# Kernel tuning notes

Hardware: AMD Instinct MI355X
Metric: run time of the kernel (lower is better)

## Reference

```python
import jax, jax.numpy as jnp
import numpy as np

H, I, SI, E = 2048, 1408, 5632, 60
B, S = 1, 512


def setup_inputs() -> dict:
    key = jax.random.key(0)
    ks = jax.random.split(key, 9)
    sc = 0.02  # weight init scale for numerical stability
    return {
        "hidden_states": jax.random.normal(ks[0], (B, S, H), dtype=jnp.float32),
        "router_w": jax.random.normal(ks[1], (E, H), dtype=jnp.float32) * sc,
        "gate_w": jax.random.normal(ks[2], (E, I, H), dtype=jnp.float32) * sc,
        "up_w": jax.random.normal(ks[3], (E, I, H), dtype=jnp.float32) * sc,
        "down_w": jax.random.normal(ks[4], (E, H, I), dtype=jnp.float32) * sc,
        "sh_gate_w": jax.random.normal(ks[5], (SI, H), dtype=jnp.float32) * sc,
        "sh_up_w": jax.random.normal(ks[6], (SI, H), dtype=jnp.float32) * sc,
        "sh_down_w": jax.random.normal(ks[7], (H, SI), dtype=jnp.float32) * sc,
        "expert_gate_w": jax.random.normal(ks[8], (1, H), dtype=jnp.float32) * sc,
        "top_k": 4,
    }


NORM_TOPK_PROB = False  # Qwen1.5-MoE config


def reference(hidden_states, router_w, gate_w, up_w, down_w,
              sh_gate_w, sh_up_w, sh_down_w, expert_gate_w, top_k):
    b, s, h = hidden_states.shape
    x = hidden_states.reshape(-1, h)                      # [T, H]

    # --- router: softmax over all experts, then top-k sparse weights ---
    logits = x @ router_w.T                               # [T, E]
    probs = jax.nn.softmax(logits.astype(jnp.float32), axis=-1)
    vals, idx = jax.lax.top_k(probs, top_k)               # [T, k]
    if NORM_TOPK_PROB:
        vals = vals / jnp.sum(vals, axis=-1, keepdims=True)
    # scatter top-k weights back to dense [T, E] (zeros elsewhere)
    onehot = jax.nn.one_hot(idx, E, dtype=probs.dtype)    # [T, k, E]
    w = jnp.einsum('tke,tk->te', onehot, vals).astype(x.dtype)  # [T, E]

    # --- grouped GLU experts (dense-masked faithful reference) ---
    g = jnp.einsum('td,eid->tei', x, gate_w)              # [T, E, I]
    a = jax.nn.silu(g) * jnp.einsum('td,eid->tei', x, up_w)
    moe = jnp.einsum('tei,ehi,te->th', a, down_w, w)      # [T, H]

    # --- shared expert with sigmoid gate ---
    shared = (jax.nn.silu(x @ sh_gate_w.T) * (x @ sh_up_w.T)) @ sh_down_w.T
    shared = jax.nn.sigmoid(x @ expert_gate_w.T) * shared # [T,1]*[T,H]

    return (moe + shared).reshape(b, s, h)
```

## Files before the change

kernel.cpp:

```cpp
#include <hip/hip_runtime.h>
#include <hip/hip_bf16.h>
#include <stdint.h>

#define TOKENS 512
#define HDIM   2048
#define IDIM   1408
#define SIDIM  5632
#define NEXP   60
#define TOPK   4
#define NSLOTS (TOKENS*TOPK)
#define ROWPAD 64

#define VMWAIT(N) asm volatile("s_waitcnt vmcnt(" #N ")" ::: "memory")
#define SBAR()    asm volatile("s_barrier" ::: "memory")

typedef __attribute__((ext_vector_type(8))) short bf16x8;
typedef __attribute__((ext_vector_type(4))) float f32x4;

__device__ __forceinline__ short f2bf(float f){
  uint32_t u = __float_as_uint(f);
  u = (u + 0x7fffu + ((u >> 16) & 1u)) >> 16;
  return (short)(u & 0xffffu);
}

__device__ __forceinline__ bf16x8 pack8(float4 a, float4 b){
  bf16x8 r;
  r[0]=f2bf(a.x); r[1]=f2bf(a.y); r[2]=f2bf(a.z); r[3]=f2bf(a.w);
  r[4]=f2bf(b.x); r[5]=f2bf(b.y); r[6]=f2bf(b.z); r[7]=f2bf(b.w);
  return r;
}

__device__ __forceinline__ bf16x8 as_bf16x8(float4 v){
  union { float4 f; bf16x8 b; } u; u.f = v; return u.b;
}

__device__ __forceinline__ f32x4 zero4(){
  f32x4 z; z[0]=0.f; z[1]=0.f; z[2]=0.f; z[3]=0.f; return z;
}

__device__ __forceinline__ f32x4 mfma16(bf16x8 a, bf16x8 b, f32x4 c){
  return __builtin_amdgcn_mfma_f32_16x16x32_bf16(a, b, c, 0, 0, 0);
}

__device__ __forceinline__ void stage_w(float4* tile, const float* __restrict__ W,
                                        int K, int k0, int tid){
  int l = tid & 63, wv = tid >> 6;
  #pragma unroll
  for (int i=0;i<4;i++){
    int r  = i*16 + wv*4 + (l>>4);
    int lu = ((l & 15) - (r & 15)) & 15;
    const float* src = W + (size_t)r*K + k0 + lu*4;
    float4* dst = tile + (size_t)(i*16 + wv*4)*16;
    __builtin_amdgcn_global_load_lds(
        (const __attribute__((address_space(1))) void*)src,
        (__attribute__((address_space(3))) void*)dst, 16, 0, 0);
  }
}

__device__ __forceinline__ void read_wfrag(const float4* tile, int r, int kq,
                                           bf16x8& b0, bf16x8& b1){
  int rot = r & 15;
  const float4* row = tile + (size_t)r*16;
  float4 f0 = row[(2*kq     + rot) & 15];
  float4 f1 = row[(2*kq + 1 + rot) & 15];
  float4 f2 = row[(2*kq + 8 + rot) & 15];
  float4 f3 = row[(2*kq + 9 + rot) & 15];
  b0 = pack8(f0, f1);
  b1 = pack8(f2, f3);
}

__device__ __forceinline__ void stage_a(float4* tile, const short* __restrict__ Arows,
                                        int K, int k0, int tid){
  int l = tid & 63, wv = tid >> 6;
  #pragma unroll
  for (int j=0;j<2;j++){
    int u0 = wv*128 + j*64;
    int u  = u0 + l;
    int row = u >> 3;
    int lu  = ((u & 7) - (row & 7)) & 7;
    const short* src = Arows + (size_t)row*K + k0 + lu*8;
    __builtin_amdgcn_global_load_lds(
        (const __attribute__((address_space(1))) void*)src,
        (__attribute__((address_space(3))) void*)(tile + u0), 16, 0, 0);
  }
}

__device__ __forceinline__ void read_afrag(const float4* tile, int c16, int kq,
                                           bf16x8* av){
  #pragma unroll
  for (int mf=0; mf<4; mf++){
    int row = c16 + 16*mf;
    const float4* rp = tile + (size_t)row*8;
    av[mf]   = as_bf16x8(rp[(kq     + row) & 7]);
    av[4+mf] = as_bf16x8(rp[(kq + 4 + row) & 7]);
  }
}

__device__ __forceinline__ void swz_decode(bool expert_mode, int& bx, int& by){
  int bid = blockIdx.y * gridDim.x + blockIdx.x;
  int nb  = gridDim.x * gridDim.y;
  int w_  = ((nb & 7) == 0) ? ((bid & 7) * (nb >> 3) + (bid >> 3)) : bid;
  if (expert_mode){ bx = w_ % gridDim.x; by = w_ / gridDim.x; }
  else            { by = w_ % gridDim.y; bx = w_ / gridDim.y; }
}

__global__ __launch_bounds__(64) void router_kernel(
    const float* __restrict__ x, const float* __restrict__ rw,
    const float* __restrict__ egw, int* __restrict__ topk_idx,
    float* __restrict__ topk_w, float* __restrict__ gates,
    int* __restrict__ counts)
{
  int t = blockIdx.x;
  int lane = threadIdx.x;
  const float* xr = x + (size_t)t*HDIM;
  float xv[HDIM/64];
  #pragma unroll
  for (int i=0;i<HDIM/64;i++) xv[i] = xr[lane + 64*i];

  float mylogit = -1e30f;
  for (int e=0;e<NEXP;e++){
    const float* w = rw + (size_t)e*HDIM;
    float acc = 0.f;
    #pragma unroll
    for (int i=0;i<HDIM/64;i++) acc += xv[i]*w[lane+64*i];
    #pragma unroll
    for (int s=32;s>0;s>>=1) acc += __shfl_xor(acc, s);
    if (lane == e) mylogit = acc;
  }
  {
    float acc = 0.f;
    #pragma unroll
    for (int i=0;i<HDIM/64;i++) acc += xv[i]*egw[lane+64*i];
    #pragma unroll
    for (int s=32;s>0;s>>=1) acc += __shfl_xor(acc, s);
    if (lane == 0) gates[t] = 1.f/(1.f + __expf(-acc));
  }
  float m = mylogit;
  #pragma unroll
  for (int s=32;s>0;s>>=1) m = fmaxf(m, __shfl_xor(m, s));
  float p = (lane < NEXP) ? __expf(mylogit - m) : 0.f;
  float sum = p;
  #pragma unroll
  for (int s=32;s>0;s>>=1) sum += __shfl_xor(sum, s);
  float prob = p / sum;
  for (int k=0;k<TOPK;k++){
    float v = prob; int idx = lane;
    #pragma unroll
    for (int s=32;s>0;s>>=1){
      float ov = __shfl_xor(v, s); int oi = __shfl_xor(idx, s);
      if (ov > v || (ov == v && oi < idx)){ v = ov; idx = oi; }
    }
    if (lane == 0){
      topk_idx[t*TOPK+k] = idx;
      topk_w[t*TOPK+k]  = v;
      atomicAdd(&counts[idx], 1);
    }
    if (lane == idx) prob = -1e30f;
  }
}

__global__ void prefix_kernel(const int* __restrict__ counts, int* __restrict__ offsets)
{
  if (threadIdx.x == 0){
    int acc = 0;
    for (int e=0;e<NEXP;e++){ offsets[e] = acc; acc += counts[e]; }
    offsets[NEXP] = acc;
  }
}

__global__ __launch_bounds__(256) void scatter_kernel(
    const float* __restrict__ x, const int* __restrict__ topk_idx,
    const int* __restrict__ offsets, int* __restrict__ fill,
    int* __restrict__ slot_of, __hip_bfloat16* __restrict__ xg,
    __hip_bfloat16* __restrict__ xb)
{
  int t = blockIdx.x, tid = threadIdx.x;
  __shared__ int sl[TOPK];
  if (tid == 0){
    for (int k=0;k<TOPK;k++){
      int e = topk_idx[t*TOPK+k];
      int pos = atomicAdd(&fill[e], 1);
      int s = offsets[e] + pos;
      slot_of[t*TOPK+k] = s;
      sl[k] = s;
    }
  }
  __syncthreads();
  const float4* xr = (const float4*)(x + (size_t)t*HDIM);
  float4 v0 = xr[tid*2], v1 = xr[tid*2+1];
  bf16x8 b = pack8(v0, v1);
  *(bf16x8*)((short*)xb + (size_t)t*HDIM + tid*8) = b;
  #pragma unroll
  for (int k=0;k<TOPK;k++)
    *(bf16x8*)((short*)xg + (size_t)sl[k]*HDIM + tid*8) = b;
}

__global__ __launch_bounds__(256) void gateup_kernel(
    const float* __restrict__ Wg_base, const float* __restrict__ Wu_base,
    const __hip_bfloat16* __restrict__ A, __hip_bfloat16* __restrict__ out,
    const int* __restrict__ offsets, int K, int NI)
{
  extern __shared__ __align__(16) char smem[];
  float4* G0 = (float4*)smem;
  float4* G1 = G0 + 1024;
  float4* U0 = G1 + 1024;
  float4* U1 = U0 + 1024;
  float4* A0 = U1 + 1024;
  float4* A1 = A0 + 512;

  int bx, by;
  swz_decode(offsets != nullptr, bx, by);

  int m_start, m_end;
  const float *Wg = Wg_base, *Wu = Wu_base;
  if (offsets){
    m_start = offsets[by]; m_end = offsets[by+1];
    size_t wo = (size_t)by * NI * K;
    Wg += wo; Wu += wo;
  } else {
    m_start = by * 64; m_end = m_start + 64;
  }
  if (m_start >= m_end) return;

  int tid  = threadIdx.x;
  int lane = tid & 63;
  int wv   = tid >> 6;
  int c16 = lane & 15, kq = lane >> 4;
  int wrow = bx*64 + wv*16 + c16;
  int r    = wv*16 + c16;
  const float* WgT = Wg + (size_t)(bx*64)*K;
  const float* WuT = Wu + (size_t)(bx*64)*K;
  const short* As = (const short*)A;

  for (int m0 = m_start; m0 < m_end; m0 += 64){
    int mrem = m_end - m0;
    const short* Ar = As + (size_t)m0*K;
    f32x4 accg[4], accu[4];
    #pragma unroll
    for (int i=0;i<4;i++){ accg[i] = zero4(); accu[i] = zero4(); }

    stage_w(G0, WgT, K, 0, tid);
    stage_w(U0, WuT, K, 0, tid);
    stage_a(A0, Ar,  K, 0, tid);

    for (int k0 = 0; k0 < K; k0 += 128){
      stage_w(G1, WgT, K, k0+64, tid);
      stage_w(U1, WuT, K, k0+64, tid);
      stage_a(A1, Ar,  K, k0+64, tid);
      VMWAIT(10); SBAR();
      {
        bf16x8 av[8], bg0,bg1,bu0,bu1;
        read_afrag(A0, c16, kq, av);
        read_wfrag(G0, r, kq, bg0, bg1);
        read_wfrag(U0, r, kq, bu0, bu1);
        #pragma unroll
        for (int mf=0; mf<4; mf++){
          accg[mf] = mfma16(av[mf],   bg0, accg[mf]);
          accu[mf] = mfma16(av[mf],   bu0, accu[mf]);
          accg[mf] = mfma16(av[4+mf], bg1, accg[mf]);
          accu[mf] = mfma16(av[4+mf], bu1, accu[mf]);
        }
      }
      SBAR();
      if (k0 + 128 < K){
        stage_w(G0, WgT, K, k0+128, tid);
        stage_w(U0, WuT, K, k0+128, tid);
        stage_a(A0, Ar,  K, k0+128, tid);
        VMWAIT(10);
      } else {
        VMWAIT(0);
      }
      SBAR();
      {
        bf16x8 av[8], bg0,bg1,bu0,bu1;
        read_afrag(A1, c16, kq, av);
        read_wfrag(G1, r, kq, bg0, bg1);
        read_wfrag(U1, r, kq, bu0, bu1);
        #pragma unroll
        for (int mf=0; mf<4; mf++){
          accg[mf] = mfma16(av[mf],   bg0, accg[mf]);
          accu[mf] = mfma16(av[mf],   bu0, accu[mf]);
          accg[mf] = mfma16(av[4+mf], bg1, accg[mf]);
          accu[mf] = mfma16(av[4+mf], bu1, accu[mf]);
        }
      }
      SBAR();
    }

    #pragma unroll
    for (int mf=0; mf<4; mf++){
      #pragma unroll
      for (int j=0;j<4;j++){
        int mrow = mf*16 + kq*4 + j;
        if (mrow < mrem){
          float g = accg[mf][j], u = accu[mf][j];
          float s = g * u / (1.f + __expf(-g));
          ((short*)out)[(size_t)(m0+mrow)*NI + wrow] = f2bf(s);
        }
      }
    }
  }
}

__global__ __launch_bounds__(256) void down_kernel(
    const float* __restrict__ W_base, const __hip_bfloat16* __restrict__ A,
    float* __restrict__ out, const int* __restrict__ offsets, int K, int NH)
{
  extern __shared__ __align__(16) char smem[];
  float4* W0 = (float4*)smem;
  float4* W1 = W0 + 1024;
  float4* A0 = W1 + 1024;
  float4* A1 = A0 + 512;

  int bx, by;
  swz_decode(offsets != nullptr, bx, by);

  int m_start, m_end;
  const float* W = W_base;
  if (offsets){
    m_start = offsets[by]; m_end = offsets[by+1];
    W += (size_t)by * NH * K;
  } else {
    m_start = by * 64; m_end = m_start + 64;
  }
  if (m_start >= m_end) return;

  int tid  = threadIdx.x;
  int lane = tid & 63;
  int wv   = tid >> 6;
  int c16 = lane & 15, kq = lane >> 4;
  int wrow = bx*64 + wv*16 + c16;
  int r    = wv*16 + c16;
  const float* WT = W + (size_t)(bx*64)*K;
  const short* As = (const short*)A;

  for (int m0 = m_start; m0 < m_end; m0 += 64){
    int mrem = m_end - m0;
    const short* Ar = As + (size_t)m0*K;
    f32x4 acc[4];
    #pragma unroll
    for (int i=0;i<4;i++) acc[i] = zero4();

    stage_w(W0, WT, K, 0, tid);
    stage_a(A0, Ar, K, 0, tid);

    for (int k0 = 0; k0 < K; k0 += 128){
      stage_w(W1, WT, K, k0+64, tid);
      stage_a(A1, Ar, K, k0+64, tid);
      VMWAIT(6); SBAR();
      {
        bf16x8 av[8], b0,b1;
        read_afrag(A0, c16, kq, av);
        read_wfrag(W0, r, kq, b0, b1);
        #pragma unroll
        for (int mf=0; mf<4; mf++){
          acc[mf] = mfma16(av[mf],   b0, acc[mf]);
          acc[mf] = mfma16(av[4+mf], b1, acc[mf]);
        }
      }
      SBAR();
      if (k0 + 128 < K){
        stage_w(W0, WT, K, k0+128, tid);
        stage_a(A0, Ar, K, k0+128, tid);
        VMWAIT(6);
      } else {
        VMWAIT(0);
      }
      SBAR();
      {
        bf16x8 av[8], b0,b1;
        read_afrag(A1, c16, kq, av);
        read_wfrag(W1, r, kq, b0, b1);
        #pragma unroll
        for (int mf=0; mf<4; mf++){
          acc[mf] = mfma16(av[mf],   b0, acc[mf]);
          acc[mf] = mfma16(av[4+mf], b1, acc[mf]);
        }
      }
      SBAR();
    }

    #pragma unroll
    for (int mf=0; mf<4; mf++){
      #pragma unroll
      for (int j=0;j<4;j++){
        int mrow = mf*16 + kq*4 + j;
        if (mrow < mrem)
          out[(size_t)(m0+mrow)*NH + wrow] = acc[mf][j];
      }
    }
  }
}

__global__ __launch_bounds__(256) void combine_kernel(
    const float* __restrict__ dslot, const float* __restrict__ shdown,
    const int* __restrict__ slot_of, const float* __restrict__ topw,
    const float* __restrict__ gates, float* __restrict__ out)
{
  int t = blockIdx.x, tid = threadIdx.x;
  int4  sl = ((const int4*)slot_of)[t];
  float4 w = ((const float4*)topw)[t];
  float sg = gates[t];
  const float* r0 = dslot + (size_t)sl.x*HDIM;
  const float* r1 = dslot + (size_t)sl.y*HDIM;
  const float* r2 = dslot + (size_t)sl.z*HDIM;
  const float* r3 = dslot + (size_t)sl.w*HDIM;
  const float* rs = shdown + (size_t)t*HDIM;
  float* o = out + (size_t)t*HDIM;
  #pragma unroll
  for (int it=0; it<HDIM/(256*4); ++it){
    int h = (tid + it*256) * 4;
    float4 a0 = *(const float4*)(r0+h);
    float4 a1 = *(const float4*)(r1+h);
    float4 a2 = *(const float4*)(r2+h);
    float4 a3 = *(const float4*)(r3+h);
    float4 as = *(const float4*)(rs+h);
    float4 r;
    r.x = w.x*a0.x + w.y*a1.x + w.z*a2.x + w.w*a3.x + sg*as.x;
    r.y = w.x*a0.y + w.y*a1.y + w.z*a2.y + w.w*a3.y + sg*as.y;
    r.z = w.x*a0.z + w.y*a1.z + w.z*a2.z + w.w*a3.z + sg*as.z;
    r.w = w.x*a0.w + w.y*a1.w + w.z*a2.w + w.w*a3.w + sg*as.w;
    *(float4*)(o+h) = r;
  }
}

extern "C" void kernel_launch(void* const* d_in, const int* in_sizes, int n_in,
                              void* d_out, int out_size, void* d_ws, size_t ws_size,
                              hipStream_t stream)
{
  const float* x         = (const float*)d_in[0];
  const float* router_w  = (const float*)d_in[1];
  const float* gate_w    = (const float*)d_in[2];
  const float* up_w      = (const float*)d_in[3];
  const float* down_w    = (const float*)d_in[4];
  const float* sh_gate_w = (const float*)d_in[5];
  const float* sh_up_w   = (const float*)d_in[6];
  const float* sh_down_w = (const float*)d_in[7];
  const float* eg_w      = (const float*)d_in[8];

  char* p = (char*)d_ws;
  auto alloc = [&](size_t bytes)->char*{
    char* r = p; p += (bytes + 255) & ~(size_t)255; return r;
  };
  int*   counts   = (int*)  alloc(NEXP*4);
  int*   fill     = (int*)  alloc(NEXP*4);
  int*   offsets  = (int*)  alloc((NEXP+1)*4);
  int*   topk_idx = (int*)  alloc(NSLOTS*4);
  float* topk_w   = (float*)alloc(NSLOTS*4);
  int*   slot_of  = (int*)  alloc(NSLOTS*4);
  float* gates    = (float*)alloc(TOKENS*4);
  __hip_bfloat16* xb    = (__hip_bfloat16*)alloc((size_t)TOKENS*HDIM*2);
  __hip_bfloat16* xg    = (__hip_bfloat16*)alloc((size_t)(NSLOTS+ROWPAD)*HDIM*2);
  __hip_bfloat16* act   = (__hip_bfloat16*)alloc((size_t)(NSLOTS+ROWPAD)*IDIM*2);
  __hip_bfloat16* shact = (__hip_bfloat16*)alloc((size_t)TOKENS*SIDIM*2);
  float* dslot  = (float*)alloc((size_t)NSLOTS*HDIM*4);
  float* shdown = (float*)alloc((size_t)TOKENS*HDIM*4);
  if ((size_t)(p - (char*)d_ws) > ws_size) return;

  hipMemsetAsync(counts, 0, NEXP*4, stream);
  hipMemsetAsync(fill,   0, NEXP*4, stream);

  router_kernel <<<TOKENS, 64, 0, stream>>>(x, router_w, eg_w, topk_idx, topk_w, gates, counts);
  prefix_kernel <<<1, 64, 0, stream>>>(counts, offsets);
  scatter_kernel<<<TOKENS, 256, 0, stream>>>(x, topk_idx, offsets, fill, slot_of, xg, xb);

  gateup_kernel<<<dim3(IDIM/64,  NEXP),     256, 80*1024, stream>>>(gate_w,    up_w,    xg,    act,   offsets, HDIM,  IDIM);
  down_kernel  <<<dim3(HDIM/64,  NEXP),     256, 48*1024, stream>>>(down_w,    act,     dslot, offsets, IDIM,  HDIM);
  gateup_kernel<<<dim3(SIDIM/64, TOKENS/64),256, 80*1024, stream>>>(sh_gate_w, sh_up_w, xb,    shact, nullptr, HDIM,  SIDIM);
  down_kernel  <<<dim3(HDIM/64,  TOKENS/64),256, 48*1024, stream>>>(sh_down_w, shact,   shdown, nullptr, SIDIM, HDIM);

  combine_kernel<<<TOKENS, 256, 0, stream>>>(dslot, shdown, slot_of, topk_w, gates, (float*)d_out);
}
```

Baseline: 666.9 us.

## Merge expert and shared GEMMs into single launches with smaller K tiles

The separate expert and shared-expert gate/up and down launches are replaced by two combined kernels. Each kernel splits its flat grid between shared-expert and routed-expert tiles, with an XCD-aware block mapping. The K step is halved from 64 to 32, which halves LDS per block (40KB and 24KB) and sets launch bounds to allow 4 blocks per CU. The aim is to remove tail idle time between launches and raise occupancy to hide weight streaming latency. In exchange there are twice as many barriers per K, and fewer MFMAs run between each barrier.

```diff
diff --git a/kernel.cpp b/kernel.cpp
--- a/kernel.cpp
+++ b/kernel.cpp
@@ -42,66 +42,50 @@
   return __builtin_amdgcn_mfma_f32_16x16x32_bf16(a, b, c, 0, 0, 0);
 }
 
-__device__ __forceinline__ void stage_w(float4* tile, const float* __restrict__ W,
-                                        int K, int k0, int tid){
+__device__ __forceinline__ void stage_w32(float4* tile, const float* __restrict__ W,
+                                          int K, int k0, int tid){
   int l = tid & 63, wv = tid >> 6;
   #pragma unroll
-  for (int i=0;i<4;i++){
-    int r  = i*16 + wv*4 + (l>>4);
-    int lu = ((l & 15) - (r & 15)) & 15;
-    const float* src = W + (size_t)r*K + k0 + lu*4;
-    float4* dst = tile + (size_t)(i*16 + wv*4)*16;
-    __builtin_amdgcn_global_load_lds(
-        (const __attribute__((address_space(1))) void*)src,
-        (__attribute__((address_space(3))) void*)dst, 16, 0, 0);
-  }
-}
-
-__device__ __forceinline__ void read_wfrag(const float4* tile, int r, int kq,
-                                           bf16x8& b0, bf16x8& b1){
-  int rot = r & 15;
-  const float4* row = tile + (size_t)r*16;
-  float4 f0 = row[(2*kq     + rot) & 15];
-  float4 f1 = row[(2*kq + 1 + rot) & 15];
-  float4 f2 = row[(2*kq + 8 + rot) & 15];
-  float4 f3 = row[(2*kq + 9 + rot) & 15];
-  b0 = pack8(f0, f1);
-  b1 = pack8(f2, f3);
-}
-
-__device__ __forceinline__ void stage_a(float4* tile, const short* __restrict__ Arows,
-                                        int K, int k0, int tid){
-  int l = tid & 63, wv = tid >> 6;
-  #pragma unroll
   for (int j=0;j<2;j++){
-    int u0 = wv*128 + j*64;
+    int u0 = j*256 + wv*64;
     int u  = u0 + l;
     int row = u >> 3;
     int lu  = ((u & 7) - (row & 7)) & 7;
-    const short* src = Arows + (size_t)row*K + k0 + lu*8;
+    const float* src = W + (size_t)row*K + k0 + lu*4;
     __builtin_amdgcn_global_load_lds(
         (const __attribute__((address_space(1))) void*)src,
         (__attribute__((address_space(3))) void*)(tile + u0), 16, 0, 0);
   }
 }
 
-__device__ __forceinline__ void read_afrag(const float4* tile, int c16, int kq,
-                                           bf16x8* av){
+__device__ __forceinline__ bf16x8 read_wfrag32(const float4* tile, int r, int kq){
+  int rot = r & 7;
+  const float4* row = tile + (size_t)r*8;
+  float4 f0 = row[(2*kq     + rot) & 7];
+  float4 f1 = row[(2*kq + 1 + rot) & 7];
+  return pack8(f0, f1);
+}
+
+__device__ __forceinline__ void stage_a32(float4* tile, const short* __restrict__ Arows,
+                                          int K, int k0, int tid){
+  int l = tid & 63, wv = tid >> 6;
+  int u0 = wv*64;
+  int u  = u0 + l;
+  int row = u >> 2;
+  int lu  = ((u & 3) - (row & 3)) & 3;
+  const short* src = Arows + (size_t)row*K + k0 + lu*8;
+  __builtin_amdgcn_global_load_lds(
+      (const __attribute__((address_space(1))) void*)src,
+      (__attribute__((address_space(3))) void*)(tile + u0), 16, 0, 0);
+}
+
+__device__ __forceinline__ void read_afrag32(const float4* tile, int c16, int kq,
+                                             bf16x8* av){
   #pragma unroll
   for (int mf=0; mf<4; mf++){
     int row = c16 + 16*mf;
-    const float4* rp = tile + (size_t)row*8;
-    av[mf]   = as_bf16x8(rp[(kq     + row) & 7]);
-    av[4+mf] = as_bf16x8(rp[(kq + 4 + row) & 7]);
-  }
-}
-
-__device__ __forceinline__ void swz_decode(bool expert_mode, int& bx, int& by){
-  int bid = blockIdx.y * gridDim.x + blockIdx.x;
-  int nb  = gridDim.x * gridDim.y;
-  int w_  = ((nb & 7) == 0) ? ((bid & 7) * (nb >> 3) + (bid >> 3)) : bid;
-  if (expert_mode){ bx = w_ % gridDim.x; by = w_ / gridDim.x; }
-  else            { by = w_ % gridDim.y; bx = w_ / gridDim.y; }
+    av[mf] = as_bf16x8(tile[(size_t)row*4 + ((kq + row) & 3)]);
+  }
 }
 
 __global__ __launch_bounds__(64) void router_kernel(
@@ -195,32 +179,41 @@
     *(bf16x8*)((short*)xg + (size_t)sl[k]*HDIM + tid*8) = b;
 }
 
-__global__ __launch_bounds__(256) void gateup_kernel(
-    const float* __restrict__ Wg_base, const float* __restrict__ Wu_base,
-    const __hip_bfloat16* __restrict__ A, __hip_bfloat16* __restrict__ out,
-    const int* __restrict__ offsets, int K, int NI)
+__global__ __launch_bounds__(256, 4) void gateup_all(
+    const float* __restrict__ gW_e, const float* __restrict__ uW_e,
+    const __hip_bfloat16* __restrict__ A_e, __hip_bfloat16* __restrict__ out_e,
+    const float* __restrict__ gW_s, const float* __restrict__ uW_s,
+    const __hip_bfloat16* __restrict__ A_s, __hip_bfloat16* __restrict__ out_s,
+    const int* __restrict__ offsets)
 {
   extern __shared__ __align__(16) char smem[];
   float4* G0 = (float4*)smem;
-  float4* G1 = G0 + 1024;
-  float4* U0 = G1 + 1024;
-  float4* U1 = U0 + 1024;
-  float4* A0 = U1 + 1024;
-  float4* A1 = A0 + 512;
-
-  int bx, by;
-  swz_decode(offsets != nullptr, bx, by);
-
-  int m_start, m_end;
-  const float *Wg = Wg_base, *Wu = Wu_base;
-  if (offsets){
-    m_start = offsets[by]; m_end = offsets[by+1];
-    size_t wo = (size_t)by * NI * K;
-    Wg += wo; Wu += wo;
+  float4* G1 = G0 + 512;
+  float4* U0 = G1 + 512;
+  float4* U1 = U0 + 512;
+  float4* A0 = U1 + 512;
+  float4* A1 = A0 + 256;
+
+  int bid = blockIdx.x;
+  int xcd = bid & 7, pos = bid >> 3;
+  const float *Wg, *Wu; const short *Abase; short *outp;
+  int NI, bx, m_start, m_end;
+  if (pos < 88){
+    bx = pos;
+    Wg = gW_s; Wu = uW_s; Abase = (const short*)A_s; outp = (short*)out_s;
+    NI = SIDIM;
+    m_start = xcd*64; m_end = m_start + 64;
   } else {
-    m_start = by * 64; m_end = m_start + 64;
+    int q = xcd*165 + (pos - 88);
+    int e = q/22; bx = q - e*22;
+    size_t wo = (size_t)e * IDIM * HDIM;
+    Wg = gW_e + wo; Wu = uW_e + wo;
+    Abase = (const short*)A_e; outp = (short*)out_e;
+    NI = IDIM;
+    m_start = offsets[e]; m_end = offsets[e+1];
   }
   if (m_start >= m_end) return;
+  const int K = HDIM;
 
   int tid  = threadIdx.x;
   int lane = tid & 63;
@@ -230,58 +223,53 @@
   int r    = wv*16 + c16;
   const float* WgT = Wg + (size_t)(bx*64)*K;
   const float* WuT = Wu + (size_t)(bx*64)*K;
-  const short* As = (const short*)A;
 
   for (int m0 = m_start; m0 < m_end; m0 += 64){
     int mrem = m_end - m0;
-    const short* Ar = As + (size_t)m0*K;
+    const short* Ar = Abase + (size_t)m0*K;
     f32x4 accg[4], accu[4];
     #pragma unroll
     for (int i=0;i<4;i++){ accg[i] = zero4(); accu[i] = zero4(); }
 
-    stage_w(G0, WgT, K, 0, tid);
-    stage_w(U0, WuT, K, 0, tid);
-    stage_a(A0, Ar,  K, 0, tid);
-
-    for (int k0 = 0; k0 < K; k0 += 128){
-      stage_w(G1, WgT, K, k0+64, tid);
-      stage_w(U1, WuT, K, k0+64, tid);
-      stage_a(A1, Ar,  K, k0+64, tid);
-      VMWAIT(10); SBAR();
+    stage_w32(G0, WgT, K, 0, tid);
+    stage_w32(U0, WuT, K, 0, tid);
+    stage_a32(A0, Ar,  K, 0, tid);
+
+    for (int k0 = 0; k0 < K; k0 += 64){
+      stage_w32(G1, WgT, K, k0+32, tid);
+      stage_w32(U1, WuT, K, k0+32, tid);
+      stage_a32(A1, Ar,  K, k0+32, tid);
+      VMWAIT(5); SBAR();
       {
-        bf16x8 av[8], bg0,bg1,bu0,bu1;
-        read_afrag(A0, c16, kq, av);
-        read_wfrag(G0, r, kq, bg0, bg1);
-        read_wfrag(U0, r, kq, bu0, bu1);
+        bf16x8 av[4];
+        read_afrag32(A0, c16, kq, av);
+        bf16x8 bg = read_wfrag32(G0, r, kq);
+        bf16x8 bu = read_wfrag32(U0, r, kq);
         #pragma unroll
         for (int mf=0; mf<4; mf++){
-          accg[mf] = mfma16(av[mf],   bg0, accg[mf]);
-          accu[mf] = mfma16(av[mf],   bu0, accu[mf]);
-          accg[mf] = mfma16(av[4+mf], bg1, accg[mf]);
-          accu[mf] = mfma16(av[4+mf], bu1, accu[mf]);
+          accg[mf] = mfma16(av[mf], bg, accg[mf]);
+          accu[mf] = mfma16(av[mf], bu, accu[mf]);
         }
       }
       SBAR();
-      if (k0 + 128 < K){
-        stage_w(G0, WgT, K, k0+128, tid);
-        stage_w(U0, WuT, K, k0+128, tid);
-        stage_a(A0, Ar,  K, k0+128, tid);
-        VMWAIT(10);
+      if (k0 + 64 < K){
+        stage_w32(G0, WgT, K, k0+64, tid);
+        stage_w32(U0, WuT, K, k0+64, tid);
+        stage_a32(A0, Ar,  K, k0+64, tid);
+        VMWAIT(5);
       } else {
         VMWAIT(0);
       }
       SBAR();
       {
-        bf16x8 av[8], bg0,bg1,bu0,bu1;
-        read_afrag(A1, c16, kq, av);
-        read_wfrag(G1, r, kq, bg0, bg1);
-        read_wfrag(U1, r, kq, bu0, bu1);
+        bf16x8 av[4];
+        read_afrag32(A1, c16, kq, av);
+        bf16x8 bg = read_wfrag32(G1, r, kq);
+        bf16x8 bu = read_wfrag32(U1, r, kq);
         #pragma unroll
         for (int mf=0; mf<4; mf++){
-          accg[mf] = mfma16(av[mf],   bg0, accg[mf]);
-          accu[mf] = mfma16(av[mf],   bu0, accu[mf]);
-          accg[mf] = mfma16(av[4+mf], bg1, accg[mf]);
-          accu[mf] = mfma16(av[4+mf], bu1, accu[mf]);
+          accg[mf] = mfma16(av[mf], bg, accg[mf]);
+          accu[mf] = mfma16(av[mf], bu, accu[mf]);
         }
       }
       SBAR();
@@ -295,33 +283,40 @@
         if (mrow < mrem){
           float g = accg[mf][j], u = accu[mf][j];
           float s = g * u / (1.f + __expf(-g));
-          ((short*)out)[(size_t)(m0+mrow)*NI + wrow] = f2bf(s);
+          outp[(size_t)(m0+mrow)*NI + wrow] = f2bf(s);
         }
       }
     }
   }
 }
 
-__global__ __launch_bounds__(256) void down_kernel(
-    const float* __restrict__ W_base, const __hip_bfloat16* __restrict__ A,
-    float* __restrict__ out, const int* __restrict__ offsets, int K, int NH)
+__global__ __launch_bounds__(256, 4) void down_all(
+    const float* __restrict__ W_e, const __hip_bfloat16* __restrict__ A_e,
+    float* __restrict__ out_e,
+    const float* __restrict__ W_s, const __hip_bfloat16* __restrict__ A_s,
+    float* __restrict__ out_s,
+    const int* __restrict__ offsets)
 {
   extern __shared__ __align__(16) char smem[];
   float4* W0 = (float4*)smem;
-  float4* W1 = W0 + 1024;
-  float4* A0 = W1 + 1024;
-  float4* A1 = A0 + 512;
-
-  int bx, by;
-  swz_decode(offsets != nullptr, bx, by);
-
-  int m_start, m_end;
-  const float* W = W_base;
-  if (offsets){
-    m_start = offsets[by]; m_end = offsets[by+1];
-    W += (size_t)by * NH * K;
+  float4* W1 = W0 + 512;
+  float4* A0 = W1 + 512;
+  float4* A1 = A0 + 256;
+
+  int bid = blockIdx.x;
+  int xcd = bid & 7, pos = bid >> 3;
+  const float* W; const short* Abase; float* outp;
+  int K, bx, m_start, m_end;
+  if (pos < 32){
+    bx = pos;
+    W = W_s; Abase = (const short*)A_s; outp = out_s; K = SIDIM;
+    m_start = xcd*64; m_end = m_start + 64;
   } else {
-    m_start = by * 64; m_end = m_start + 64;
+    int q = xcd*240 + (pos - 32);
+    int e = q >> 5; bx = q & 31;
+    W = W_e + (size_t)e * HDIM * IDIM;
+    Abase = (const short*)A_e; outp = out_e; K = IDIM;
+    m_start = offsets[e]; m_end = offsets[e+1];
   }
   if (m_start >= m_end) return;
 
@@ -332,50 +327,45 @@
   int wrow = bx*64 + wv*16 + c16;
   int r    = wv*16 + c16;
   const float* WT = W + (size_t)(bx*64)*K;
-  const short* As = (const short*)A;
 
   for (int m0 = m_start; m0 < m_end; m0 += 64){
     int mrem = m_end - m0;
-    const short* Ar = As + (size_t)m0*K;
+    const short* Ar = Abase + (size_t)m0*K;
     f32x4 acc[4];
     #pragma unroll
     for (int i=0;i<4;i++) acc[i] = zero4();
 
-    stage_w(W0, WT, K, 0, tid);
-    stage_a(A0, Ar, K, 0, tid);
-
-    for (int k0 = 0; k0 < K; k0 += 128){
-      stage_w(W1, WT, K, k0+64, tid);
-      stage_a(A1, Ar, K, k0+64, tid);
-      VMWAIT(6); SBAR();
+    stage_w32(W0, WT, K, 0, tid);
+    stage_a32(A0, Ar, K, 0, tid);
+
+    for (int k0 = 0; k0 < K; k0 += 64){
+      stage_w32(W1, WT, K, k0+32, tid);
+      stage_a32(A1, Ar, K, k0+32, tid);
+      VMWAIT(3); SBAR();
       {
-        bf16x8 av[8], b0,b1;
-        read_afrag(A0, c16, kq, av);
-        read_wfrag(W0, r, kq, b0, b1);
+        bf16x8 av[4];
+        read_afrag32(A0, c16, kq, av);
+        bf16x8 b = read_wfrag32(W0, r, kq);
         #pragma unroll
-        for (int mf=0; mf<4; mf++){
-          acc[mf] = mfma16(av[mf],   b0, acc[mf]);
-          acc[mf] = mfma16(av[4+mf], b1, acc[mf]);
-        }
-      }
-      SBAR();
-      if (k0 + 128 < K){
-        stage_w(W0, WT, K, k0+128, tid);
-        stage_a(A0, Ar, K, k0+128, tid);
-        VMWAIT(6);
+        for (int mf=0; mf<4; mf++)
+          acc[mf] = mfma16(av[mf], b, acc[mf]);
+      }
+      SBAR();
+      if (k0 + 64 < K){
+        stage_w32(W0, WT, K, k0+64, tid);
+        stage_a32(A0, Ar, K, k0+64, tid);
+        VMWAIT(3);
       } else {
         VMWAIT(0);
       }
       SBAR();
       {
-        bf16x8 av[8], b0,b1;
-        read_afrag(A1, c16, kq, av);
-        read_wfrag(W1, r, kq, b0, b1);
+        bf16x8 av[4];
+        read_afrag32(A1, c16, kq, av);
+        bf16x8 b = read_wfrag32(W1, r, kq);
         #pragma unroll
-        for (int mf=0; mf<4; mf++){
-          acc[mf] = mfma16(av[mf],   b0, acc[mf]);
-          acc[mf] = mfma16(av[4+mf], b1, acc[mf]);
-        }
+        for (int mf=0; mf<4; mf++)
+          acc[mf] = mfma16(av[mf], b, acc[mf]);
       }
       SBAR();
     }
@@ -386,7 +376,7 @@
       for (int j=0;j<4;j++){
         int mrow = mf*16 + kq*4 + j;
         if (mrow < mrem)
-          out[(size_t)(m0+mrow)*NH + wrow] = acc[mf][j];
+          outp[(size_t)(m0+mrow)*HDIM + wrow] = acc[mf][j];
       }
     }
   }
@@ -464,10 +454,13 @@
   prefix_kernel <<<1, 64, 0, stream>>>(counts, offsets);
   scatter_kernel<<<TOKENS, 256, 0, stream>>>(x, topk_idx, offsets, fill, slot_of, xg, xb);
 
-  gateup_kernel<<<dim3(IDIM/64,  NEXP),     256, 80*1024, stream>>>(gate_w,    up_w,    xg,    act,   offsets, HDIM,  IDIM);
-  down_kernel  <<<dim3(HDIM/64,  NEXP),     256, 48*1024, stream>>>(down_w,    act,     dslot, offsets, IDIM,  HDIM);
-  gateup_kernel<<<dim3(SIDIM/64, TOKENS/64),256, 80*1024, stream>>>(sh_gate_w, sh_up_w, xb,    shact, nullptr, HDIM,  SIDIM);
-  down_kernel  <<<dim3(HDIM/64,  TOKENS/64),256, 48*1024, stream>>>(sh_down_w, shact,   shdown, nullptr, SIDIM, HDIM);
+  gateup_all<<<2024, 256, 40*1024, stream>>>(
+      gate_w, up_w, xg, act,
+      sh_gate_w, sh_up_w, xb, shact, offsets);
+
+  down_all<<<2176, 256, 24*1024, stream>>>(
+      down_w, act, dslot,
+      sh_down_w, shact, shdown, offsets);
 
   combine_kernel<<<TOKENS, 256, 0, stream>>>(dslot, shdown, slot_of, topk_w, gates, (float*)d_out);
 }
```

New measurement: 654.1 us. No clear change (-1.9%).
